# Performance work log

Hardware: AMD Instinct MI355X
Metric: run time of the kernel (lower is better)

Reference implementation:

```python
import jax, jax.numpy as jnp
import numpy as np
import math

B, S, D = 2, 2048, 1024
H, HD = 16, 64
ROT = 16          # rotary_dim = head_dim * 0.25
FF = 4096
EPS = 1e-5


def setup_inputs() -> dict:
    key = jax.random.key(0)
    ks = jax.random.split(key, 12)
    sc = lambda *sh: 0.02
    inp = {
        "x": jax.random.normal(ks[0], (B, S, D), jnp.float32),
        "attention_mask": jnp.tril(jnp.ones((S, S), bool))[None, None],  # causal [1,1,S,S]
        "W_qkv": jax.random.normal(ks[1], (3 * D, D), jnp.float32) * 0.02,
        "b_qkv": jnp.zeros((3 * D,), jnp.float32),
        "W_o": jax.random.normal(ks[2], (D, D), jnp.float32) * 0.02,
        "b_o": jnp.zeros((D,), jnp.float32),
        "ln1_w": jnp.ones((D,), jnp.float32),
        "ln1_b": jnp.zeros((D,), jnp.float32),
        "ln2_w": jnp.ones((D,), jnp.float32),
        "ln2_b": jnp.zeros((D,), jnp.float32),
        "W1": jax.random.normal(ks[3], (FF, D), jnp.float32) * 0.02,
        "b1": jnp.zeros((FF,), jnp.float32),
        "W2": jax.random.normal(ks[4], (D, FF), jnp.float32) * 0.02,
        "b2": jnp.zeros((D,), jnp.float32),
    }
    # real rotary frequencies, shaped [1,1,S,ROT//2,2]
    inv_freq = 1.0 / (10000.0 ** (jnp.arange(0, ROT, 2, dtype=jnp.float32) / ROT))
    t = jnp.arange(S, dtype=jnp.float32)
    ang = t[:, None] * inv_freq[None, :]                      # [S, ROT//2]
    inp["freqs_cis"] = jnp.stack([jnp.cos(ang), jnp.sin(ang)], -1)[None, None]
    return inp


def layer_norm(x, w, b):
    mu = jnp.mean(x, -1, keepdims=True)
    var = jnp.mean(jnp.square(x - mu), -1, keepdims=True)
    return (x - mu) * jax.lax.rsqrt(var + EPS) * w + b


def apply_rotate_emb(x, freqs_cis):
    # x: [B,H,S,ROT]; freqs_cis: [1,1,S,ROT//2,2]
    x1, x2 = x[..., : ROT // 2], x[..., ROT // 2 :]
    cos, sin = freqs_cis[..., 0], freqs_cis[..., 1]
    return jnp.concatenate([x1 * cos - x2 * sin, x1 * sin + x2 * cos], -1)


def reference(x, attention_mask, freqs_cis, W_qkv, b_qkv, W_o, b_o,
              ln1_w, ln1_b, ln2_w, ln2_b, W1, b1, W2, b2):
    h = layer_norm(x, ln1_w, ln1_b)
    qkv = jnp.einsum("bsd,ed->bse", h, W_qkv) + b_qkv
    q, k, v = jnp.split(qkv, 3, axis=-1)
    to_heads = lambda t: t.reshape(B, S, H, HD).transpose(0, 2, 1, 3)  # [B,H,S,HD]
    q, k, v = to_heads(q), to_heads(k), to_heads(v)
    q = jnp.concatenate([apply_rotate_emb(q[..., :ROT], freqs_cis), q[..., ROT:]], -1)
    k = jnp.concatenate([apply_rotate_emb(k[..., :ROT], freqs_cis), k[..., ROT:]], -1)
    scores = jnp.einsum("bhqd,bhkd->bhqk", q, k) / math.sqrt(HD)
    scores = jnp.where(attention_mask, scores, -jnp.inf)
    probs = jax.nn.softmax(scores, axis=-1)
    out = jnp.einsum("bhqk,bhkd->bhqd", probs, v)
    out = out.transpose(0, 2, 1, 3).reshape(B, S, D)
    attn_out = jnp.einsum("bsd,ed->bse", out, W_o) + b_o
    # parallel residual (dropout is identity in eval)
    h2 = layer_norm(x, ln2_w, ln2_b)
    ff = jnp.einsum("bsf,df->bsd", jax.nn.gelu(jnp.einsum("bsd,fd->bsf", h2, W1) + b1, approximate=False), W2) + b2
    return x + ff + attn_out
```

## Files before the change

kernel.cpp:

```cpp
#include <hip/hip_runtime.h>

#define DEV __device__ __forceinline__

typedef __bf16 bf16;
typedef bf16 bf16x4 __attribute__((ext_vector_type(4)));
typedef bf16 bf16x8 __attribute__((ext_vector_type(8)));
typedef float f32x4 __attribute__((ext_vector_type(4)));

DEV f32x4 mfma16(bf16x8 a, bf16x8 b, f32x4 c) {
  return __builtin_amdgcn_mfma_f32_16x16x32_bf16(a, b, c, 0, 0, 0);
}

DEV void gload_lds16(const bf16* g, bf16* l) {
  __builtin_amdgcn_global_load_lds((const __attribute__((address_space(1))) void*)g,
                                   (__attribute__((address_space(3))) void*)l, 16, 0, 0);
}

#define PH_BAR __builtin_amdgcn_s_barrier()
#define VM(NSTR) asm volatile("s_waitcnt vmcnt(" NSTR ")" ::: "memory")
#define WAITBAR(NSTR) asm volatile("s_waitcnt vmcnt(" NSTR ")\n\ts_barrier" ::: "memory")

DEV float fast_gelu(float x) {
  const float z = x * x;
  const float w = __builtin_fmaf(z, 0.1029353f, 2.3019853f);
  const float e = __builtin_amdgcn_exp2f(x * w);
  const float r = __builtin_amdgcn_rcpf(1.0f + e);
  return x - x * r;
}

__global__ __launch_bounds__(256) void ln_cast_all(
    const float* __restrict__ x,
    const float* __restrict__ ln1w, const float* __restrict__ ln1b,
    const float* __restrict__ ln2w, const float* __restrict__ ln2b,
    bf16* __restrict__ h1, bf16* __restrict__ h2,
    const float* __restrict__ Wqkv_f, const float* __restrict__ W1_f,
    const float* __restrict__ Wo_f, const float* __restrict__ W2_f,
    bf16* __restrict__ wQKV, bf16* __restrict__ w1, bf16* __restrict__ wCat)
{
  const int b = blockIdx.x, t = threadIdx.x;
  if (b < 4096) {
    __shared__ float red[2][4];
    const int lane = t & 63, wave = t >> 6;
    const float4 v = ((const float4*)(x + (size_t)b * 1024))[t];
    float vv[4] = {v.x, v.y, v.z, v.w};
    float s = vv[0] + vv[1] + vv[2] + vv[3];
    float q = vv[0]*vv[0] + vv[1]*vv[1] + vv[2]*vv[2] + vv[3]*vv[3];
    #pragma unroll
    for (int o = 32; o; o >>= 1) { s += __shfl_xor(s, o); q += __shfl_xor(q, o); }
    if (lane == 0) { red[0][wave] = s; red[1][wave] = q; }
    __syncthreads();
    s = red[0][0] + red[0][1] + red[0][2] + red[0][3];
    q = red[1][0] + red[1][1] + red[1][2] + red[1][3];
    const float mu = s * (1.0f / 1024.0f);
    const float var = q * (1.0f / 1024.0f) - mu * mu;
    const float rs = rsqrtf(var + 1e-5f);
    bf16x4 o1, o2;
    #pragma unroll
    for (int j = 0; j < 4; ++j) {
      const int i = t * 4 + j;
      const float xh = (vv[j] - mu) * rs;
      o1[j] = (bf16)(xh * ln1w[i] + ln1b[i]);
      o2[j] = (bf16)(xh * ln2w[i] + ln2b[i]);
    }
    *(bf16x4*)&h1[(size_t)b * 1024 + t * 4] = o1;
    *(bf16x4*)&h2[(size_t)b * 1024 + t * 4] = o2;
    return;
  }
  const int cb = b - 4096;
  if (cb < 3072) {
    const int i = cb * 256 + t;
    const float4 v = ((const float4*)Wqkv_f)[i];
    bf16x4 o = {(bf16)v.x, (bf16)v.y, (bf16)v.z, (bf16)v.w};
    ((bf16x4*)wQKV)[i] = o;
  } else if (cb < 7168) {
    const int i = (cb - 3072) * 256 + t;
    const float4 v = ((const float4*)W1_f)[i];
    bf16x4 o = {(bf16)v.x, (bf16)v.y, (bf16)v.z, (bf16)v.w};
    ((bf16x4*)w1)[i] = o;
  } else if (cb < 8192) {
    const int row = cb - 7168;
    const float4 v = *(const float4*)&Wo_f[(size_t)row * 1024 + t * 4];
    bf16x4 o = {(bf16)v.x, (bf16)v.y, (bf16)v.z, (bf16)v.w};
    *(bf16x4*)&wCat[(size_t)row * 5120 + t * 4] = o;
  } else {
    const int row = cb - 8192;
    #pragma unroll
    for (int k = 0; k < 4; ++k) {
      const int col = t * 4 + k * 1024;
      const float4 v = *(const float4*)&W2_f[(size_t)row * 4096 + col];
      bf16x4 o = {(bf16)v.x, (bf16)v.y, (bf16)v.z, (bf16)v.w};
      *(bf16x4*)&wCat[(size_t)row * 5120 + 1024 + col] = o;
    }
  }
}

DEV bf16x8 ldfrag(const bf16* unit, int lr, int g) {
  return *(const bf16x8*)&unit[lr * 32 + ((g ^ ((lr >> 1) & 3)) << 3)];
}
DEV void read_bfr(const bf16* unit, int blr, int g, bf16x8 bfr[4]) {
  #pragma unroll
  for (int nj = 0; nj < 4; ++nj) bfr[nj] = ldfrag(unit, blr + nj * 16, g);
}
DEV void read_af(const bf16* unit, int alr, int g, bf16x8 af[4]) {
  #pragma unroll
  for (int ml = 0; ml < 4; ++ml) af[ml] = ldfrag(unit, alr + ml * 16, g);
}
DEV void do_mfma(const bf16x8 af[4], const bf16x8 bfr[4], f32x4 acc[8][4], int mh) {
  __builtin_amdgcn_s_setprio(1);
  #pragma unroll
  for (int ml = 0; ml < 4; ++ml)
    #pragma unroll
    for (int nj = 0; nj < 4; ++nj)
      acc[mh * 4 + ml][nj] = mfma16(af[ml], bfr[nj], acc[mh * 4 + ml][nj]);
  __builtin_amdgcn_s_setprio(0);
}

template <int EPI>
__global__ __launch_bounds__(512) void gemm256(
    const bf16* __restrict__ A, const bf16* __restrict__ B,
    const float* __restrict__ bias, void* __restrict__ Cv,
    void* __restrict__ P1, void* __restrict__ P2, void* __restrict__ P3,
    int K, int ldc, int ntiles, int nbx, int nkt)
{
  __shared__ __align__(16) bf16 As[2][2][2][4096];
  __shared__ __align__(16) bf16 Bs[2][2][2][4096];
  const int tid = threadIdx.x;
  const int lane = tid & 63, wave = tid >> 6;
  const int wm = wave >> 2, wn = wave & 3;
  const int g = lane >> 4, c = lane & 15;
  const int cpx = gridDim.x >> 3;
  const int swz = ((int)blockIdx.x & 7) * cpx + ((int)blockIdx.x >> 3);
  const int tile = swz % ntiles;
  const int sk = swz / ntiles;
  const int bm = (tile / nbx) * 256, bn = (tile % nbx) * 256;

  const int slr = tid >> 2;
  const int sch = (tid & 3) ^ ((tid >> 3) & 3);
  const bf16* aU[2][2];
  const bf16* bU[2][2];
  {
    const bf16* a0 = A + (size_t)(bm + ((slr >> 6) * 128) + (slr & 63)) * K
                       + (size_t)sk * nkt * 64 + sch * 8;
    const bf16* b0 = B + (size_t)(bn + slr) * K + (size_t)sk * nkt * 64 + sch * 8;
    aU[0][0] = a0;            aU[0][1] = a0 + (size_t)64 * K;
    aU[1][0] = a0 + 32;       aU[1][1] = a0 + (size_t)64 * K + 32;
    bU[0][0] = b0;            bU[0][1] = b0 + (size_t)128 * K;
    bU[1][0] = b0 + 32;       bU[1][1] = b0 + (size_t)128 * K + 32;
  }
#define STG_A(bf_, kkh_, ub_, ko_) gload_lds16(aU[kkh_][ub_] + (ko_), &As[bf_][kkh_][ub_][wave * 512])
#define STG_B(bf_, kkh_, ub_, ko_) gload_lds16(bU[kkh_][ub_] + (ko_), &Bs[bf_][kkh_][ub_][wave * 512])

  f32x4 acc[8][4] = {};
  bf16x8 bfr[4], af[4];
  const int alr = (wm << 6) + c;
  const int blr = ((wn & 1) << 6) + c;
  const int bub = wn >> 1;

  STG_B(0, 0, 0, 0); STG_B(0, 0, 1, 0); STG_A(0, 0, 0, 0); STG_A(0, 0, 1, 0);
  STG_B(0, 1, 0, 0); STG_B(0, 1, 1, 0); STG_A(0, 1, 0, 0); STG_A(0, 1, 1, 0);
  WAITBAR("4");

  for (int t = 0; t < nkt - 1; ++t) {
    const int buf = t & 1, nxt = buf ^ 1;
    const int ko = (t + 1) * 64;
    read_bfr(&Bs[buf][0][bub][0], blr, g, bfr);
    read_af(&As[buf][0][0][0], alr, g, af);
    STG_B(nxt, 0, 0, ko); STG_B(nxt, 0, 1, ko);
    PH_BAR;
    do_mfma(af, bfr, acc, 0);
    PH_BAR;
    read_af(&As[buf][0][1][0], alr, g, af);
    STG_A(nxt, 0, 0, ko); STG_A(nxt, 0, 1, ko);
    PH_BAR;
    do_mfma(af, bfr, acc, 1);
    VM("4");
    PH_BAR;
    read_bfr(&Bs[buf][1][bub][0], blr, g, bfr);
    read_af(&As[buf][1][0][0], alr, g, af);
    STG_B(nxt, 1, 0, ko); STG_B(nxt, 1, 1, ko);
    PH_BAR;
    do_mfma(af, bfr, acc, 0);
    PH_BAR;
    read_af(&As[buf][1][1][0], alr, g, af);
    STG_A(nxt, 1, 0, ko); STG_A(nxt, 1, 1, ko);
    PH_BAR;
    do_mfma(af, bfr, acc, 1);
    VM("4");
    PH_BAR;
  }
  {
    const int buf = (nkt - 1) & 1;
    read_bfr(&Bs[buf][0][bub][0], blr, g, bfr);
    read_af(&As[buf][0][0][0], alr, g, af);
    PH_BAR;
    do_mfma(af, bfr, acc, 0);
    PH_BAR;
    read_af(&As[buf][0][1][0], alr, g, af);
    PH_BAR;
    do_mfma(af, bfr, acc, 1);
    VM("0");
    PH_BAR;
    read_bfr(&Bs[buf][1][bub][0], blr, g, bfr);
    read_af(&As[buf][1][0][0], alr, g, af);
    PH_BAR;
    do_mfma(af, bfr, acc, 0);
    PH_BAR;
    read_af(&As[buf][1][1][0], alr, g, af);
    PH_BAR;
    do_mfma(af, bfr, acc, 1);
  }
#undef STG_A
#undef STG_B

  bf16* Pp = nullptr;
  if constexpr (EPI == 2)
    Pp = (bf16*)((sk == 1) ? P1 : (sk == 2) ? P2 : (sk == 3) ? P3 : Cv);
  const int row0 = bm + wm * 128 + 4 * g;
  const int col0 = bn + wn * 64 + c;
  #pragma unroll
  for (int mi = 0; mi < 8; ++mi) {
    #pragma unroll
    for (int nj = 0; nj < 4; ++nj) {
      const int col = col0 + nj * 16;
      float bv = 0.0f;
      if constexpr (EPI < 2) bv = bias[col];
      #pragma unroll
      for (int r = 0; r < 4; ++r) {
        const size_t idx = (size_t)(row0 + mi * 16 + r) * ldc + col;
        float vo = acc[mi][nj][r] + bv;
        if constexpr (EPI == 0) {
          ((bf16*)Cv)[idx] = (bf16)vo;
        } else if constexpr (EPI == 1) {
          ((bf16*)Cv)[idx] = (bf16)fast_gelu(vo);
        } else {
          Pp[idx] = (bf16)vo;
        }
      }
    }
  }
}

__global__ __launch_bounds__(256) void combine_out(
    const bf16* __restrict__ q0, const bf16* __restrict__ q1,
    const bf16* __restrict__ q2, const bf16* __restrict__ q3,
    const float* __restrict__ x,
    const float* __restrict__ bo, const float* __restrict__ b2,
    float* __restrict__ out)
{
  const int row = blockIdx.x, t = threadIdx.x;
  const size_t base = (size_t)row * 1024 + t * 4;
  const bf16x4 a0 = *(const bf16x4*)&q0[base];
  const bf16x4 a1 = *(const bf16x4*)&q1[base];
  const bf16x4 a2 = *(const bf16x4*)&q2[base];
  const bf16x4 a3 = *(const bf16x4*)&q3[base];
  const float4 vx = *(const float4*)&x[base];
  const float4 vb = *(const float4*)&bo[t * 4];
  const float4 vc = *(const float4*)&b2[t * 4];
  float4 o;
  o.x = (float)a0[0] + (float)a1[0] + (float)a2[0] + (float)a3[0] + vx.x + vb.x + vc.x;
  o.y = (float)a0[1] + (float)a1[1] + (float)a2[1] + (float)a3[1] + vx.y + vb.y + vc.y;
  o.z = (float)a0[2] + (float)a1[2] + (float)a2[2] + (float)a3[2] + vx.z + vb.z + vc.z;
  o.w = (float)a0[3] + (float)a1[3] + (float)a2[3] + (float)a3[3] + vx.w + vb.w + vc.w;
  *(float4*)&out[base] = o;
}

__global__ __launch_bounds__(256) void rope_reshape(
    const bf16* __restrict__ qkv, const float* __restrict__ freqs,
    bf16* __restrict__ Q, bf16* __restrict__ K, bf16* __restrict__ VT)
{
  __shared__ bf16 vt[64][72];
  const int t = threadIdx.x;
  const int bh = blockIdx.y, b = bh >> 4, h = bh & 15;
  const int sc = blockIdx.x * 64;
  const int sl = t >> 2, s = sc + sl;
  const int d0 = (t & 3) * 16;

  const size_t rowbase = (size_t)(b * 2048 + s) * 3072 + h * 64 + d0;
  const size_t obase = ((size_t)bh * 2048 + s) * 64 + d0;

  #pragma unroll
  for (int which = 0; which < 2; ++which) {
    const bf16* src = qkv + rowbase + which * 1024;
    bf16x8 v0 = *(const bf16x8*)src;
    bf16x8 v1 = *(const bf16x8*)(src + 8);
    if (d0 == 0) {
      bf16x8 r0, r1;
      #pragma unroll
      for (int j = 0; j < 8; ++j) {
        const float cs = freqs[s * 16 + j * 2];
        const float sn = freqs[s * 16 + j * 2 + 1];
        const float x1 = (float)v0[j], x2 = (float)v1[j];
        r0[j] = (bf16)(x1 * cs - x2 * sn);
        r1[j] = (bf16)(x1 * sn + x2 * cs);
      }
      v0 = r0; v1 = r1;
    }
    bf16* dst = (which == 0 ? Q : K) + obase;
    *(bf16x8*)dst = v0;
    *(bf16x8*)(dst + 8) = v1;
  }
  {
    const bf16* src = qkv + rowbase + 2048;
    bf16x8 v0 = *(const bf16x8*)src;
    bf16x8 v1 = *(const bf16x8*)(src + 8);
    #pragma unroll
    for (int j = 0; j < 8; ++j) { vt[sl][d0 + j] = v0[j]; vt[sl][d0 + 8 + j] = v1[j]; }
  }
  __syncthreads();
  {
    const int d = t >> 2;
    const int s0 = (t & 3) * 16;
    bf16x8 o0, o1;
    #pragma unroll
    for (int j = 0; j < 8; ++j) { o0[j] = vt[s0 + j][d]; o1[j] = vt[s0 + 8 + j][d]; }
    bf16* dst = VT + ((size_t)bh * 64 + d) * 2048 + sc + s0;
    *(bf16x8*)dst = o0;
    *(bf16x8*)(dst + 8) = o1;
  }
}

__global__ __launch_bounds__(512, 4) void attn_kernel(
    const bf16* __restrict__ Q, const bf16* __restrict__ Kg,
    const bf16* __restrict__ VTg, bf16* __restrict__ O, int ldO)
{
  __shared__ __align__(16) bf16 Ks[4][64][64];
  __shared__ __align__(16) bf16 Vs[4][64][64];
  __shared__ __align__(16) bf16 Ps[8][16][64];

  const int tid = threadIdx.x;
  const int lane = tid & 63, wave = tid >> 6;
  const int g = lane >> 4, c = lane & 15;
  const int L = blockIdx.x;
  const int half = L >> 8, r = L & 255;
  const int bh = (half << 4) | (r >> 4);
  const int qtile = half ? (15 - (r & 15)) : (r & 15);
  const int qw = qtile * 128 + wave * 16;

  const bf16* Qp = Q + (size_t)bh * 2048 * 64;
  const bf16* Kp = Kg + (size_t)bh * 2048 * 64;
  const bf16* Vp = VTg + (size_t)bh * 64 * 2048;

  const int srow = lane >> 3;
  const int schunk = (lane & 7) ^ srow;
  const int svr = wave * 8 + srow;
  const size_t kdelta = (size_t)64 * 64;

  bf16x8 qreg[2];
  {
    const float qs = 0.125f * 1.44269504f;
    bf16x8 t0 = *(const bf16x8*)&Qp[(size_t)(qw + c) * 64 + g * 8];
    bf16x8 t1 = *(const bf16x8*)&Qp[(size_t)(qw + c) * 64 + 32 + g * 8];
    #pragma unroll
    for (int j = 0; j < 8; ++j) {
      qreg[0][j] = (bf16)((float)t0[j] * qs);
      qreg[1][j] = (bf16)((float)t1[j] * qs);
    }
  }
  bf16x8 ones;
  #pragma unroll
  for (int j = 0; j < 8; ++j) ones[j] = (bf16)1.0f;

  const int cq = c & 7;
  int fo[4][2];
  #pragma unroll
  for (int i = 0; i < 4; ++i)
    #pragma unroll
    for (int kk = 0; kk < 2; ++kk)
      fo[i][kk] = (i * 16 + c) * 64 + (((kk * 4 + g) ^ cq) << 3);
  bf16* pw[4];
  #pragma unroll
  for (int kf = 0; kf < 4; ++kf)
    pw[kf] = &Ps[wave][c][((((kf * 2 + (g >> 1)) ^ cq) << 3)) + ((g & 1) << 2)];
  const bf16* pr[2];
  #pragma unroll
  for (int kk = 0; kk < 2; ++kk)
    pr[kk] = &Ps[wave][c][((kk * 4 + g) ^ cq) << 3];
  const bf16* ks0 = &Ks[0][0][0];
  const bf16* vs0 = &Vs[0][0][0];

  f32x4 oacc[4] = {};
  f32x4 lacc = {};
  float m_ = -1e30f;

  const int nkb = 2 * qtile + 2;
#define STAGE(j_) do { const int b4_ = (j_) & 3;                                   \
    gload_lds16(&Kp[(size_t)((j_) * 64 + svr) * 64 + schunk * 8], &Ks[b4_][wave * 8][0]); \
    gload_lds16(&Vp[(size_t)svr * 2048 + (j_) * 64 + schunk * 8], &Vs[b4_][wave * 8][0]); \
  } while (0)

  auto qkt = [&](f32x4* st, int bufi) {
    const bf16* kt = ks0 + bufi * kdelta;
    __builtin_amdgcn_s_setprio(1);
    #pragma unroll
    for (int kf = 0; kf < 4; ++kf) {
      f32x4 z = {};
      z = mfma16(*(const bf16x8*)(kt + fo[kf][0]), qreg[0], z);
      st[kf] = mfma16(*(const bf16x8*)(kt + fo[kf][1]), qreg[1], z);
    }
    __builtin_amdgcn_s_setprio(0);
  };

  auto smpv = [&](const f32x4* st, int j_, int bufi) {
    const int kbase = j_ * 64;
    float v[16];
    if (kbase + 63 > qw) {
      const int qrel = qw + c - kbase;
      #pragma unroll
      for (int kf = 0; kf < 4; ++kf)
        #pragma unroll
        for (int rr = 0; rr < 4; ++rr)
          v[kf * 4 + rr] = (kf * 16 + 4 * g + rr <= qrel) ? st[kf][rr] : -1e30f;
    } else {
      #pragma unroll
      for (int kf = 0; kf < 4; ++kf)
        #pragma unroll
        for (int rr = 0; rr < 4; ++rr)
          v[kf * 4 + rr] = st[kf][rr];
    }
    float u0 = fmaxf(fmaxf(v[0], v[1]), v[2]);
    float u1 = fmaxf(fmaxf(v[3], v[4]), v[5]);
    float u2 = fmaxf(fmaxf(v[6], v[7]), v[8]);
    float u3 = fmaxf(fmaxf(v[9], v[10]), v[11]);
    float u4 = fmaxf(fmaxf(v[12], v[13]), v[14]);
    float tm = fmaxf(fmaxf(fmaxf(u0, u1), u2), fmaxf(fmaxf(u3, u4), v[15]));
    if (__any(tm > m_ + 8.0f)) {
      float tr = fmaxf(tm, __shfl_xor(tm, 16));
      tr = fmaxf(tr, __shfl_xor(tr, 32));
      const float mn = fmaxf(m_, tr);
      const float alpha = __builtin_amdgcn_exp2f(m_ - mn);
      m_ = mn;
      lacc[0] *= alpha; lacc[1] *= alpha; lacc[2] *= alpha; lacc[3] *= alpha;
      #pragma unroll
      for (int df = 0; df < 4; ++df) {
        oacc[df][0] *= alpha; oacc[df][1] *= alpha;
        oacc[df][2] *= alpha; oacc[df][3] *= alpha;
      }
    }
    bf16 p[16];
    #pragma unroll
    for (int i = 0; i < 16; ++i)
      p[i] = (bf16)__builtin_amdgcn_exp2f(v[i] - m_);
    #pragma unroll
    for (int kf = 0; kf < 4; ++kf) {
      bf16x4 pk = {p[kf * 4], p[kf * 4 + 1], p[kf * 4 + 2], p[kf * 4 + 3]};
      *(bf16x4*)pw[kf] = pk;
    }
    bf16x8 pfrag0 = *(const bf16x8*)pr[0];
    bf16x8 pfrag1 = *(const bf16x8*)pr[1];
    const bf16* vt = vs0 + bufi * kdelta;
    __builtin_amdgcn_s_setprio(1);
    #pragma unroll
    for (int df = 0; df < 4; ++df) {
      oacc[df] = mfma16(*(const bf16x8*)(vt + fo[df][0]), pfrag0, oacc[df]);
      oacc[df] = mfma16(*(const bf16x8*)(vt + fo[df][1]), pfrag1, oacc[df]);
    }
    lacc = mfma16(ones, pfrag0, lacc);
    lacc = mfma16(ones, pfrag1, lacc);
    __builtin_amdgcn_s_setprio(0);
  };

  f32x4 stA[4], stB[4];
  STAGE(0); STAGE(1); STAGE(2);
  VM("2");
  PH_BAR;
  qkt(stA, 0);

  const int nit = nkb >> 1;
  for (int i = 0; i < nit; ++i) {
    const int jA = 2 * i, jB = 2 * i + 1;
    const bool stgA = (jA + 3 < nkb);
    if (stgA) STAGE(jA + 3);
    if (jB * 64 <= qw + 15) qkt(stB, jB & 3);
    smpv(stA, jA, jA & 3);
    if (stgA) { VM("2"); } else { VM("0"); }
    PH_BAR;
    const bool stgB = (jB + 3 < nkb);
    if (stgB) STAGE(jB + 3);
    if (jB + 1 < nkb && (jB + 1) * 64 <= qw + 15) qkt(stA, (jB + 1) & 3);
    if (jB * 64 <= qw + 15) smpv(stB, jB, jB & 3);
    if (stgB) { VM("2"); } else { VM("0"); }
    PH_BAR;
  }
#undef STAGE

  const int b = bh >> 4, h = bh & 15;
  const float inv = 1.0f / lacc[0];
  const int s = qw + c;
  #pragma unroll
  for (int df = 0; df < 4; ++df) {
    bf16x4 o;
    #pragma unroll
    for (int rr = 0; rr < 4; ++rr) o[rr] = (bf16)(oacc[df][rr] * inv);
    *(bf16x4*)&O[(size_t)(b * 2048 + s) * ldO + h * 64 + df * 16 + 4 * g] = o;
  }
}

extern "C" void kernel_launch(void* const* d_in, const int* in_sizes, int n_in,
                              void* d_out, int out_size, void* d_ws, size_t ws_size,
                              hipStream_t stream) {
  const float* x     = (const float*)d_in[0];
  const float* W_qkv = (const float*)d_in[2];
  const float* b_qkv = (const float*)d_in[3];
  const float* W_o   = (const float*)d_in[4];
  const float* b_o   = (const float*)d_in[5];
  const float* ln1w  = (const float*)d_in[6];
  const float* ln1b  = (const float*)d_in[7];
  const float* ln2w  = (const float*)d_in[8];
  const float* ln2b  = (const float*)d_in[9];
  const float* W1    = (const float*)d_in[10];
  const float* b1    = (const float*)d_in[11];
  const float* W2    = (const float*)d_in[12];
  const float* b2    = (const float*)d_in[13];
  const float* freqs = (const float*)d_in[14];
  float* out = (float*)d_out;

  char* ws = (char*)d_ws;
  const size_t MB = (size_t)1 << 20;
  bf16* h1   = (bf16*)(ws + 0 * MB);
  bf16* h2   = (bf16*)(ws + 8 * MB);
  bf16* wQKV = (bf16*)(ws + 16 * MB);
  bf16* wCat = (bf16*)(ws + 22 * MB);
  bf16* w1   = (bf16*)(ws + 32 * MB);
  bf16* qkv  = (bf16*)(ws + 40 * MB);
  bf16* Qb   = (bf16*)(ws + 64 * MB);
  bf16* Kb   = (bf16*)(ws + 72 * MB);
  bf16* VTb  = (bf16*)(ws + 80 * MB);
  bf16* A2   = (bf16*)(ws + 88 * MB);
  bf16* q0   = (bf16*)(ws + 0 * MB);
  bf16* q1   = (bf16*)(ws + 8 * MB);
  bf16* q2   = (bf16*)(ws + 40 * MB);
  bf16* q3   = (bf16*)(ws + 48 * MB);

  ln_cast_all<<<13312, 256, 0, stream>>>(x, ln1w, ln1b, ln2w, ln2b, h1, h2,
                                         W_qkv, W1, W_o, W2, wQKV, w1, wCat);

  gemm256<0><<<192, 512, 0, stream>>>(h1, wQKV, b_qkv, qkv,
                                      nullptr, nullptr, nullptr,
                                      1024, 3072, 192, 12, 16);
  rope_reshape<<<dim3(32, 32), 256, 0, stream>>>(qkv, freqs, Qb, Kb, VTb);
  attn_kernel<<<512, 512, 0, stream>>>(Qb, Kb, VTb, A2, 5120);
  gemm256<1><<<256, 512, 0, stream>>>(h2, w1, b1, A2 + 1024,
                                      nullptr, nullptr, nullptr,
                                      1024, 5120, 256, 16, 16);
  gemm256<2><<<256, 512, 0, stream>>>(A2, wCat, nullptr, q0,
                                      q1, q2, q3,
                                      5120, 1024, 64, 4, 20);
  combine_out<<<4096, 256, 0, stream>>>(q0, q1, q2, q3, x, b_o, b2, out);
}
```

Baseline: 196.4 us.

## Merge QKV and FFN-up GEMMs into one launch; widen attention blocks

The QKV projection and the FFN up-projection GEMMs become a single 448-block launch that picks its operands and epilogue (bias, or bias plus GELU) per block segment. This fills more CUs at once and drops a launch and a tail. The attention kernel moves from 512-thread blocks over 128 query rows to 1024-thread blocks over 256 query rows, with K and V staging split between the two thread halves. The change risks load imbalance, since causal work now varies more per block and there are only 256 attention blocks, and it adds pressure on registers and LDS.

```diff
diff --git a/kernel.cpp b/kernel.cpp
--- a/kernel.cpp
+++ b/kernel.cpp
@@ -115,11 +115,142 @@
   __builtin_amdgcn_s_setprio(0);
 }
 
-template <int EPI>
-__global__ __launch_bounds__(512) void gemm256(
+DEV void gemm_kloop(bf16 (*As)[2][2][4096], bf16 (*Bs)[2][2][4096],
+                    const bf16* aU[2][2], const bf16* bU[2][2],
+                    int wave, int alr, int blr, int bub, int g, int nkt,
+                    f32x4 acc[8][4])
+{
+  bf16x8 bfr[4], af[4];
+#define STG_A(bf_, kkh_, ub_, ko_) gload_lds16(aU[kkh_][ub_] + (ko_), &As[bf_][kkh_][ub_][wave * 512])
+#define STG_B(bf_, kkh_, ub_, ko_) gload_lds16(bU[kkh_][ub_] + (ko_), &Bs[bf_][kkh_][ub_][wave * 512])
+  STG_B(0, 0, 0, 0); STG_B(0, 0, 1, 0); STG_A(0, 0, 0, 0); STG_A(0, 0, 1, 0);
+  STG_B(0, 1, 0, 0); STG_B(0, 1, 1, 0); STG_A(0, 1, 0, 0); STG_A(0, 1, 1, 0);
+  WAITBAR("4");
+
+  for (int t = 0; t < nkt - 1; ++t) {
+    const int buf = t & 1, nxt = buf ^ 1;
+    const int ko = (t + 1) * 64;
+    read_bfr(&Bs[buf][0][bub][0], blr, g, bfr);
+    read_af(&As[buf][0][0][0], alr, g, af);
+    STG_B(nxt, 0, 0, ko); STG_B(nxt, 0, 1, ko);
+    PH_BAR;
+    do_mfma(af, bfr, acc, 0);
+    PH_BAR;
+    read_af(&As[buf][0][1][0], alr, g, af);
+    STG_A(nxt, 0, 0, ko); STG_A(nxt, 0, 1, ko);
+    PH_BAR;
+    do_mfma(af, bfr, acc, 1);
+    VM("4");
+    PH_BAR;
+    read_bfr(&Bs[buf][1][bub][0], blr, g, bfr);
+    read_af(&As[buf][1][0][0], alr, g, af);
+    STG_B(nxt, 1, 0, ko); STG_B(nxt, 1, 1, ko);
+    PH_BAR;
+    do_mfma(af, bfr, acc, 0);
+    PH_BAR;
+    read_af(&As[buf][1][1][0], alr, g, af);
+    STG_A(nxt, 1, 0, ko); STG_A(nxt, 1, 1, ko);
+    PH_BAR;
+    do_mfma(af, bfr, acc, 1);
+    VM("4");
+    PH_BAR;
+  }
+  {
+    const int buf = (nkt - 1) & 1;
+    read_bfr(&Bs[buf][0][bub][0], blr, g, bfr);
+    read_af(&As[buf][0][0][0], alr, g, af);
+    PH_BAR;
+    do_mfma(af, bfr, acc, 0);
+    PH_BAR;
+    read_af(&As[buf][0][1][0], alr, g, af);
+    PH_BAR;
+    do_mfma(af, bfr, acc, 1);
+    VM("0");
+    PH_BAR;
+    read_bfr(&Bs[buf][1][bub][0], blr, g, bfr);
+    read_af(&As[buf][1][0][0], alr, g, af);
+    PH_BAR;
+    do_mfma(af, bfr, acc, 0);
+    PH_BAR;
+    read_af(&As[buf][1][1][0], alr, g, af);
+    PH_BAR;
+    do_mfma(af, bfr, acc, 1);
+  }
+#undef STG_A
+#undef STG_B
+}
+
+__global__ __launch_bounds__(512) void gemm_dual(
+    const bf16* __restrict__ A0, const bf16* __restrict__ B0,
+    const float* __restrict__ bias0, bf16* __restrict__ C0,
+    const bf16* __restrict__ A1, const bf16* __restrict__ B1,
+    const float* __restrict__ bias1, bf16* __restrict__ C1)
+{
+  __shared__ __align__(16) bf16 As[2][2][2][4096];
+  __shared__ __align__(16) bf16 Bs[2][2][2][4096];
+  const int tid = threadIdx.x;
+  const int lane = tid & 63, wave = tid >> 6;
+  const int wm = wave >> 2, wn = wave & 3;
+  const int g = lane >> 4, c = lane & 15;
+
+  const int bid = blockIdx.x;
+  const int seg = (bid >= 192);
+  const int nseg = seg ? 256 : 192;
+  const int nbx  = seg ? 16 : 12;
+  const int ldc  = seg ? 5120 : 3072;
+  const bf16* A = seg ? A1 : A0;
+  const bf16* B = seg ? B1 : B0;
+  const float* bias = seg ? bias1 : bias0;
+  bf16* C = seg ? C1 : C0;
+  const int K = 1024, nkt = 16;
+
+  const int bs = bid - (seg ? 192 : 0);
+  const int cpx = nseg >> 3;
+  const int swz = (bs & 7) * cpx + (bs >> 3);
+  const int bm = (swz / nbx) * 256, bn = (swz % nbx) * 256;
+
+  const int slr = tid >> 2;
+  const int sch = (tid & 3) ^ ((tid >> 3) & 3);
+  const bf16* aU[2][2];
+  const bf16* bU[2][2];
+  {
+    const bf16* a0 = A + (size_t)(bm + ((slr >> 6) * 128) + (slr & 63)) * K + sch * 8;
+    const bf16* b0 = B + (size_t)(bn + slr) * K + sch * 8;
+    aU[0][0] = a0;            aU[0][1] = a0 + (size_t)64 * K;
+    aU[1][0] = a0 + 32;       aU[1][1] = a0 + (size_t)64 * K + 32;
+    bU[0][0] = b0;            bU[0][1] = b0 + (size_t)128 * K;
+    bU[1][0] = b0 + 32;       bU[1][1] = b0 + (size_t)128 * K + 32;
+  }
+
+  f32x4 acc[8][4] = {};
+  const int alr = (wm << 6) + c;
+  const int blr = ((wn & 1) << 6) + c;
+  const int bub = wn >> 1;
+
+  gemm_kloop(As, Bs, aU, bU, wave, alr, blr, bub, g, nkt, acc);
+
+  const int row0 = bm + wm * 128 + 4 * g;
+  const int col0 = bn + wn * 64 + c;
+  #pragma unroll
+  for (int mi = 0; mi < 8; ++mi) {
+    #pragma unroll
+    for (int nj = 0; nj < 4; ++nj) {
+      const int col = col0 + nj * 16;
+      const float bv = bias[col];
+      #pragma unroll
+      for (int r = 0; r < 4; ++r) {
+        const size_t idx = (size_t)(row0 + mi * 16 + r) * ldc + col;
+        const float vo = acc[mi][nj][r] + bv;
+        C[idx] = (bf16)(seg ? fast_gelu(vo) : vo);
+      }
+    }
+  }
+}
+
+__global__ __launch_bounds__(512) void gemm_splitk(
     const bf16* __restrict__ A, const bf16* __restrict__ B,
-    const float* __restrict__ bias, void* __restrict__ Cv,
-    void* __restrict__ P1, void* __restrict__ P2, void* __restrict__ P3,
+    bf16* __restrict__ P0, bf16* __restrict__ P1,
+    bf16* __restrict__ P2, bf16* __restrict__ P3,
     int K, int ldc, int ntiles, int nbx, int nkt)
 {
   __shared__ __align__(16) bf16 As[2][2][2][4096];
@@ -147,74 +278,15 @@
     bU[0][0] = b0;            bU[0][1] = b0 + (size_t)128 * K;
     bU[1][0] = b0 + 32;       bU[1][1] = b0 + (size_t)128 * K + 32;
   }
-#define STG_A(bf_, kkh_, ub_, ko_) gload_lds16(aU[kkh_][ub_] + (ko_), &As[bf_][kkh_][ub_][wave * 512])
-#define STG_B(bf_, kkh_, ub_, ko_) gload_lds16(bU[kkh_][ub_] + (ko_), &Bs[bf_][kkh_][ub_][wave * 512])
 
   f32x4 acc[8][4] = {};
-  bf16x8 bfr[4], af[4];
   const int alr = (wm << 6) + c;
   const int blr = ((wn & 1) << 6) + c;
   const int bub = wn >> 1;
 
-  STG_B(0, 0, 0, 0); STG_B(0, 0, 1, 0); STG_A(0, 0, 0, 0); STG_A(0, 0, 1, 0);
-  STG_B(0, 1, 0, 0); STG_B(0, 1, 1, 0); STG_A(0, 1, 0, 0); STG_A(0, 1, 1, 0);
-  WAITBAR("4");
-
-  for (int t = 0; t < nkt - 1; ++t) {
-    const int buf = t & 1, nxt = buf ^ 1;
-    const int ko = (t + 1) * 64;
-    read_bfr(&Bs[buf][0][bub][0], blr, g, bfr);
-    read_af(&As[buf][0][0][0], alr, g, af);
-    STG_B(nxt, 0, 0, ko); STG_B(nxt, 0, 1, ko);
-    PH_BAR;
-    do_mfma(af, bfr, acc, 0);
-    PH_BAR;
-    read_af(&As[buf][0][1][0], alr, g, af);
-    STG_A(nxt, 0, 0, ko); STG_A(nxt, 0, 1, ko);
-    PH_BAR;
-    do_mfma(af, bfr, acc, 1);
-    VM("4");
-    PH_BAR;
-    read_bfr(&Bs[buf][1][bub][0], blr, g, bfr);
-    read_af(&As[buf][1][0][0], alr, g, af);
-    STG_B(nxt, 1, 0, ko); STG_B(nxt, 1, 1, ko);
-    PH_BAR;
-    do_mfma(af, bfr, acc, 0);
-    PH_BAR;
-    read_af(&As[buf][1][1][0], alr, g, af);
-    STG_A(nxt, 1, 0, ko); STG_A(nxt, 1, 1, ko);
-    PH_BAR;
-    do_mfma(af, bfr, acc, 1);
-    VM("4");
-    PH_BAR;
-  }
-  {
-    const int buf = (nkt - 1) & 1;
-    read_bfr(&Bs[buf][0][bub][0], blr, g, bfr);
-    read_af(&As[buf][0][0][0], alr, g, af);
-    PH_BAR;
-    do_mfma(af, bfr, acc, 0);
-    PH_BAR;
-    read_af(&As[buf][0][1][0], alr, g, af);
-    PH_BAR;
-    do_mfma(af, bfr, acc, 1);
-    VM("0");
-    PH_BAR;
-    read_bfr(&Bs[buf][1][bub][0], blr, g, bfr);
-    read_af(&As[buf][1][0][0], alr, g, af);
-    PH_BAR;
-    do_mfma(af, bfr, acc, 0);
-    PH_BAR;
-    read_af(&As[buf][1][1][0], alr, g, af);
-    PH_BAR;
-    do_mfma(af, bfr, acc, 1);
-  }
-#undef STG_A
-#undef STG_B
-
-  bf16* Pp = nullptr;
-  if constexpr (EPI == 2)
-    Pp = (bf16*)((sk == 1) ? P1 : (sk == 2) ? P2 : (sk == 3) ? P3 : Cv);
+  gemm_kloop(As, Bs, aU, bU, wave, alr, blr, bub, g, nkt, acc);
+
+  bf16* Pp = (sk == 1) ? P1 : (sk == 2) ? P2 : (sk == 3) ? P3 : P0;
   const int row0 = bm + wm * 128 + 4 * g;
   const int col0 = bn + wn * 64 + c;
   #pragma unroll
@@ -222,19 +294,10 @@
     #pragma unroll
     for (int nj = 0; nj < 4; ++nj) {
       const int col = col0 + nj * 16;
-      float bv = 0.0f;
-      if constexpr (EPI < 2) bv = bias[col];
       #pragma unroll
       for (int r = 0; r < 4; ++r) {
         const size_t idx = (size_t)(row0 + mi * 16 + r) * ldc + col;
-        float vo = acc[mi][nj][r] + bv;
-        if constexpr (EPI == 0) {
-          ((bf16*)Cv)[idx] = (bf16)vo;
-        } else if constexpr (EPI == 1) {
-          ((bf16*)Cv)[idx] = (bf16)fast_gelu(vo);
-        } else {
-          Pp[idx] = (bf16)vo;
-        }
+        Pp[idx] = (bf16)acc[mi][nj][r];
       }
     }
   }
@@ -319,30 +382,29 @@
   }
 }
 
-__global__ __launch_bounds__(512, 4) void attn_kernel(
+__global__ __launch_bounds__(1024, 4) void attn_kernel(
     const bf16* __restrict__ Q, const bf16* __restrict__ Kg,
     const bf16* __restrict__ VTg, bf16* __restrict__ O, int ldO)
 {
   __shared__ __align__(16) bf16 Ks[4][64][64];
   __shared__ __align__(16) bf16 Vs[4][64][64];
-  __shared__ __align__(16) bf16 Ps[8][16][64];
+  __shared__ __align__(16) bf16 Ps[16][16][64];
 
   const int tid = threadIdx.x;
   const int lane = tid & 63, wave = tid >> 6;
   const int g = lane >> 4, c = lane & 15;
   const int L = blockIdx.x;
-  const int half = L >> 8, r = L & 255;
-  const int bh = (half << 4) | (r >> 4);
-  const int qtile = half ? (15 - (r & 15)) : (r & 15);
-  const int qw = qtile * 128 + wave * 16;
+  const int bh = L >> 3, p = L & 7;
+  const int qw = p * 256 + wave * 16;
 
   const bf16* Qp = Q + (size_t)bh * 2048 * 64;
   const bf16* Kp = Kg + (size_t)bh * 2048 * 64;
   const bf16* Vp = VTg + (size_t)bh * 64 * 2048;
 
+  const int stw = (tid >> 6) & 7;
   const int srow = lane >> 3;
   const int schunk = (lane & 7) ^ srow;
-  const int svr = wave * 8 + srow;
+  const int svr = stw * 8 + srow;
   const size_t kdelta = (size_t)64 * 64;
 
   bf16x8 qreg[2];
@@ -382,10 +444,12 @@
   f32x4 lacc = {};
   float m_ = -1e30f;
 
-  const int nkb = 2 * qtile + 2;
-#define STAGE(j_) do { const int b4_ = (j_) & 3;                                   \
-    gload_lds16(&Kp[(size_t)((j_) * 64 + svr) * 64 + schunk * 8], &Ks[b4_][wave * 8][0]); \
-    gload_lds16(&Vp[(size_t)svr * 2048 + (j_) * 64 + schunk * 8], &Vs[b4_][wave * 8][0]); \
+  const int nkb = 4 * p + 4;
+#define STAGE(j_) do { const int b4_ = (j_) & 3;                                     \
+    if (tid < 512)                                                                   \
+      gload_lds16(&Kp[(size_t)((j_) * 64 + svr) * 64 + schunk * 8], &Ks[b4_][stw * 8][0]); \
+    else                                                                             \
+      gload_lds16(&Vp[(size_t)svr * 2048 + (j_) * 64 + schunk * 8], &Vs[b4_][stw * 8][0]); \
   } while (0)
 
   auto qkt = [&](f32x4* st, int bufi) {
@@ -436,13 +500,13 @@
         oacc[df][2] *= alpha; oacc[df][3] *= alpha;
       }
     }
-    bf16 p[16];
+    bf16 pq[16];
     #pragma unroll
     for (int i = 0; i < 16; ++i)
-      p[i] = (bf16)__builtin_amdgcn_exp2f(v[i] - m_);
+      pq[i] = (bf16)__builtin_amdgcn_exp2f(v[i] - m_);
     #pragma unroll
     for (int kf = 0; kf < 4; ++kf) {
-      bf16x4 pk = {p[kf * 4], p[kf * 4 + 1], p[kf * 4 + 2], p[kf * 4 + 3]};
+      bf16x4 pk = {pq[kf * 4], pq[kf * 4 + 1], pq[kf * 4 + 2], pq[kf * 4 + 3]};
       *(bf16x4*)pw[kf] = pk;
     }
     bf16x8 pfrag0 = *(const bf16x8*)pr[0];
@@ -461,7 +525,7 @@
 
   f32x4 stA[4], stB[4];
   STAGE(0); STAGE(1); STAGE(2);
-  VM("2");
+  VM("1");
   PH_BAR;
   qkt(stA, 0);
 
@@ -471,14 +535,14 @@
     const bool stgA = (jA + 3 < nkb);
     if (stgA) STAGE(jA + 3);
     if (jB * 64 <= qw + 15) qkt(stB, jB & 3);
-    smpv(stA, jA, jA & 3);
-    if (stgA) { VM("2"); } else { VM("0"); }
+    if (jA * 64 <= qw + 15) smpv(stA, jA, jA & 3);
+    if (stgA) { VM("1"); } else { VM("0"); }
     PH_BAR;
     const bool stgB = (jB + 3 < nkb);
     if (stgB) STAGE(jB + 3);
     if (jB + 1 < nkb && (jB + 1) * 64 <= qw + 15) qkt(stA, (jB + 1) & 3);
     if (jB * 64 <= qw + 15) smpv(stB, jB, jB & 3);
-    if (stgB) { VM("2"); } else { VM("0"); }
+    if (stgB) { VM("1"); } else { VM("0"); }
     PH_BAR;
   }
 #undef STAGE
@@ -533,17 +597,11 @@
 
   ln_cast_all<<<13312, 256, 0, stream>>>(x, ln1w, ln1b, ln2w, ln2b, h1, h2,
                                          W_qkv, W1, W_o, W2, wQKV, w1, wCat);
-
-  gemm256<0><<<192, 512, 0, stream>>>(h1, wQKV, b_qkv, qkv,
-                                      nullptr, nullptr, nullptr,
-                                      1024, 3072, 192, 12, 16);
+  gemm_dual<<<448, 512, 0, stream>>>(h1, wQKV, b_qkv, qkv,
+                                     h2, w1, b1, A2 + 1024);
   rope_reshape<<<dim3(32, 32), 256, 0, stream>>>(qkv, freqs, Qb, Kb, VTb);
-  attn_kernel<<<512, 512, 0, stream>>>(Qb, Kb, VTb, A2, 5120);
-  gemm256<1><<<256, 512, 0, stream>>>(h2, w1, b1, A2 + 1024,
-                                      nullptr, nullptr, nullptr,
-                                      1024, 5120, 256, 16, 16);
-  gemm256<2><<<256, 512, 0, stream>>>(A2, wCat, nullptr, q0,
-                                      q1, q2, q3,
-                                      5120, 1024, 64, 4, 20);
+  attn_kernel<<<256, 1024, 0, stream>>>(Qb, Kb, VTb, A2, 5120);
+  gemm_splitk<<<256, 512, 0, stream>>>(A2, wCat, q0, q1, q2, q3,
+                                       5120, 1024, 64, 4, 20);
   combine_out<<<4096, 256, 0, stream>>>(q0, q1, q2, q3, x, b_o, b2, out);
 }
```

Result: slower. 204.0 us (+3.8%).

## Use 1024-thread attention blocks covering 256 queries with split K/V staging

Applied to the files above, without the earlier changes.

The attention kernel now launches 256 blocks of 16 waves, each covering 256 query rows, instead of 512 blocks of 8 waves with paired q-tiles for causal balance. K and V staging is split so the first half of the threads loads K and the second half loads V, which changes the vmcnt waits. A guard skips fully masked softmax/PV steps per wave. The GEMM k-loop is also moved into a helper function. The new mapping drops the causal load-balancing pairing, so later query blocks do much more work than early ones, and the larger blocks may limit occupancy.

```diff
diff --git a/kernel.cpp b/kernel.cpp
--- a/kernel.cpp
+++ b/kernel.cpp
@@ -115,6 +115,71 @@
   __builtin_amdgcn_s_setprio(0);
 }
 
+DEV void gemm_kloop(bf16 (*As)[2][2][4096], bf16 (*Bs)[2][2][4096],
+                    const bf16* aU[2][2], const bf16* bU[2][2],
+                    int wave, int alr, int blr, int bub, int g, int nkt,
+                    f32x4 acc[8][4])
+{
+  bf16x8 bfr[4], af[4];
+#define STG_A(bf_, kkh_, ub_, ko_) gload_lds16(aU[kkh_][ub_] + (ko_), &As[bf_][kkh_][ub_][wave * 512])
+#define STG_B(bf_, kkh_, ub_, ko_) gload_lds16(bU[kkh_][ub_] + (ko_), &Bs[bf_][kkh_][ub_][wave * 512])
+  STG_B(0, 0, 0, 0); STG_B(0, 0, 1, 0); STG_A(0, 0, 0, 0); STG_A(0, 0, 1, 0);
+  STG_B(0, 1, 0, 0); STG_B(0, 1, 1, 0); STG_A(0, 1, 0, 0); STG_A(0, 1, 1, 0);
+  WAITBAR("4");
+
+  for (int t = 0; t < nkt - 1; ++t) {
+    const int buf = t & 1, nxt = buf ^ 1;
+    const int ko = (t + 1) * 64;
+    read_bfr(&Bs[buf][0][bub][0], blr, g, bfr);
+    read_af(&As[buf][0][0][0], alr, g, af);
+    STG_B(nxt, 0, 0, ko); STG_B(nxt, 0, 1, ko);
+    PH_BAR;
+    do_mfma(af, bfr, acc, 0);
+    PH_BAR;
+    read_af(&As[buf][0][1][0], alr, g, af);
+    STG_A(nxt, 0, 0, ko); STG_A(nxt, 0, 1, ko);
+    PH_BAR;
+    do_mfma(af, bfr, acc, 1);
+    VM("4");
+    PH_BAR;
+    read_bfr(&Bs[buf][1][bub][0], blr, g, bfr);
+    read_af(&As[buf][1][0][0], alr, g, af);
+    STG_B(nxt, 1, 0, ko); STG_B(nxt, 1, 1, ko);
+    PH_BAR;
+    do_mfma(af, bfr, acc, 0);
+    PH_BAR;
+    read_af(&As[buf][1][1][0], alr, g, af);
+    STG_A(nxt, 1, 0, ko); STG_A(nxt, 1, 1, ko);
+    PH_BAR;
+    do_mfma(af, bfr, acc, 1);
+    VM("4");
+    PH_BAR;
+  }
+  {
+    const int buf = (nkt - 1) & 1;
+    read_bfr(&Bs[buf][0][bub][0], blr, g, bfr);
+    read_af(&As[buf][0][0][0], alr, g, af);
+    PH_BAR;
+    do_mfma(af, bfr, acc, 0);
+    PH_BAR;
+    read_af(&As[buf][0][1][0], alr, g, af);
+    PH_BAR;
+    do_mfma(af, bfr, acc, 1);
+    VM("0");
+    PH_BAR;
+    read_bfr(&Bs[buf][1][bub][0], blr, g, bfr);
+    read_af(&As[buf][1][0][0], alr, g, af);
+    PH_BAR;
+    do_mfma(af, bfr, acc, 0);
+    PH_BAR;
+    read_af(&As[buf][1][1][0], alr, g, af);
+    PH_BAR;
+    do_mfma(af, bfr, acc, 1);
+  }
+#undef STG_A
+#undef STG_B
+}
+
 template <int EPI>
 __global__ __launch_bounds__(512) void gemm256(
     const bf16* __restrict__ A, const bf16* __restrict__ B,
@@ -147,70 +212,13 @@
     bU[0][0] = b0;            bU[0][1] = b0 + (size_t)128 * K;
     bU[1][0] = b0 + 32;       bU[1][1] = b0 + (size_t)128 * K + 32;
   }
-#define STG_A(bf_, kkh_, ub_, ko_) gload_lds16(aU[kkh_][ub_] + (ko_), &As[bf_][kkh_][ub_][wave * 512])
-#define STG_B(bf_, kkh_, ub_, ko_) gload_lds16(bU[kkh_][ub_] + (ko_), &Bs[bf_][kkh_][ub_][wave * 512])
 
   f32x4 acc[8][4] = {};
-  bf16x8 bfr[4], af[4];
   const int alr = (wm << 6) + c;
   const int blr = ((wn & 1) << 6) + c;
   const int bub = wn >> 1;
 
-  STG_B(0, 0, 0, 0); STG_B(0, 0, 1, 0); STG_A(0, 0, 0, 0); STG_A(0, 0, 1, 0);
-  STG_B(0, 1, 0, 0); STG_B(0, 1, 1, 0); STG_A(0, 1, 0, 0); STG_A(0, 1, 1, 0);
-  WAITBAR("4");
-
-  for (int t = 0; t < nkt - 1; ++t) {
-    const int buf = t & 1, nxt = buf ^ 1;
-    const int ko = (t + 1) * 64;
-    read_bfr(&Bs[buf][0][bub][0], blr, g, bfr);
-    read_af(&As[buf][0][0][0], alr, g, af);
-    STG_B(nxt, 0, 0, ko); STG_B(nxt, 0, 1, ko);
-    PH_BAR;
-    do_mfma(af, bfr, acc, 0);
-    PH_BAR;
-    read_af(&As[buf][0][1][0], alr, g, af);
-    STG_A(nxt, 0, 0, ko); STG_A(nxt, 0, 1, ko);
-    PH_BAR;
-    do_mfma(af, bfr, acc, 1);
-    VM("4");
-    PH_BAR;
-    read_bfr(&Bs[buf][1][bub][0], blr, g, bfr);
-    read_af(&As[buf][1][0][0], alr, g, af);
-    STG_B(nxt, 1, 0, ko); STG_B(nxt, 1, 1, ko);
-    PH_BAR;
-    do_mfma(af, bfr, acc, 0);
-    PH_BAR;
-    read_af(&As[buf][1][1][0], alr, g, af);
-    STG_A(nxt, 1, 0, ko); STG_A(nxt, 1, 1, ko);
-    PH_BAR;
-    do_mfma(af, bfr, acc, 1);
-    VM("4");
-    PH_BAR;
-  }
-  {
-    const int buf = (nkt - 1) & 1;
-    read_bfr(&Bs[buf][0][bub][0], blr, g, bfr);
-    read_af(&As[buf][0][0][0], alr, g, af);
-    PH_BAR;
-    do_mfma(af, bfr, acc, 0);
-    PH_BAR;
-    read_af(&As[buf][0][1][0], alr, g, af);
-    PH_BAR;
-    do_mfma(af, bfr, acc, 1);
-    VM("0");
-    PH_BAR;
-    read_bfr(&Bs[buf][1][bub][0], blr, g, bfr);
-    read_af(&As[buf][1][0][0], alr, g, af);
-    PH_BAR;
-    do_mfma(af, bfr, acc, 0);
-    PH_BAR;
-    read_af(&As[buf][1][1][0], alr, g, af);
-    PH_BAR;
-    do_mfma(af, bfr, acc, 1);
-  }
-#undef STG_A
-#undef STG_B
+  gemm_kloop(As, Bs, aU, bU, wave, alr, blr, bub, g, nkt, acc);
 
   bf16* Pp = nullptr;
   if constexpr (EPI == 2)
@@ -319,30 +327,29 @@
   }
 }
 
-__global__ __launch_bounds__(512, 4) void attn_kernel(
+__global__ __launch_bounds__(1024, 4) void attn_kernel(
     const bf16* __restrict__ Q, const bf16* __restrict__ Kg,
     const bf16* __restrict__ VTg, bf16* __restrict__ O, int ldO)
 {
   __shared__ __align__(16) bf16 Ks[4][64][64];
   __shared__ __align__(16) bf16 Vs[4][64][64];
-  __shared__ __align__(16) bf16 Ps[8][16][64];
+  __shared__ __align__(16) bf16 Ps[16][16][64];
 
   const int tid = threadIdx.x;
   const int lane = tid & 63, wave = tid >> 6;
   const int g = lane >> 4, c = lane & 15;
   const int L = blockIdx.x;
-  const int half = L >> 8, r = L & 255;
-  const int bh = (half << 4) | (r >> 4);
-  const int qtile = half ? (15 - (r & 15)) : (r & 15);
-  const int qw = qtile * 128 + wave * 16;
+  const int bh = L >> 3, p = L & 7;
+  const int qw = p * 256 + wave * 16;
 
   const bf16* Qp = Q + (size_t)bh * 2048 * 64;
   const bf16* Kp = Kg + (size_t)bh * 2048 * 64;
   const bf16* Vp = VTg + (size_t)bh * 64 * 2048;
 
+  const int stw = (tid >> 6) & 7;
   const int srow = lane >> 3;
   const int schunk = (lane & 7) ^ srow;
-  const int svr = wave * 8 + srow;
+  const int svr = stw * 8 + srow;
   const size_t kdelta = (size_t)64 * 64;
 
   bf16x8 qreg[2];
@@ -382,10 +389,12 @@
   f32x4 lacc = {};
   float m_ = -1e30f;
 
-  const int nkb = 2 * qtile + 2;
-#define STAGE(j_) do { const int b4_ = (j_) & 3;                                   \
-    gload_lds16(&Kp[(size_t)((j_) * 64 + svr) * 64 + schunk * 8], &Ks[b4_][wave * 8][0]); \
-    gload_lds16(&Vp[(size_t)svr * 2048 + (j_) * 64 + schunk * 8], &Vs[b4_][wave * 8][0]); \
+  const int nkb = 4 * p + 4;
+#define STAGE(j_) do { const int b4_ = (j_) & 3;                                     \
+    if (tid < 512)                                                                   \
+      gload_lds16(&Kp[(size_t)((j_) * 64 + svr) * 64 + schunk * 8], &Ks[b4_][stw * 8][0]); \
+    else                                                                             \
+      gload_lds16(&Vp[(size_t)svr * 2048 + (j_) * 64 + schunk * 8], &Vs[b4_][stw * 8][0]); \
   } while (0)
 
   auto qkt = [&](f32x4* st, int bufi) {
@@ -436,13 +445,13 @@
         oacc[df][2] *= alpha; oacc[df][3] *= alpha;
       }
     }
-    bf16 p[16];
+    bf16 pq[16];
     #pragma unroll
     for (int i = 0; i < 16; ++i)
-      p[i] = (bf16)__builtin_amdgcn_exp2f(v[i] - m_);
+      pq[i] = (bf16)__builtin_amdgcn_exp2f(v[i] - m_);
     #pragma unroll
     for (int kf = 0; kf < 4; ++kf) {
-      bf16x4 pk = {p[kf * 4], p[kf * 4 + 1], p[kf * 4 + 2], p[kf * 4 + 3]};
+      bf16x4 pk = {pq[kf * 4], pq[kf * 4 + 1], pq[kf * 4 + 2], pq[kf * 4 + 3]};
       *(bf16x4*)pw[kf] = pk;
     }
     bf16x8 pfrag0 = *(const bf16x8*)pr[0];
@@ -461,7 +470,7 @@
 
   f32x4 stA[4], stB[4];
   STAGE(0); STAGE(1); STAGE(2);
-  VM("2");
+  VM("1");
   PH_BAR;
   qkt(stA, 0);
 
@@ -471,14 +480,14 @@
     const bool stgA = (jA + 3 < nkb);
     if (stgA) STAGE(jA + 3);
     if (jB * 64 <= qw + 15) qkt(stB, jB & 3);
-    smpv(stA, jA, jA & 3);
-    if (stgA) { VM("2"); } else { VM("0"); }
+    if (jA * 64 <= qw + 15) smpv(stA, jA, jA & 3);
+    if (stgA) { VM("1"); } else { VM("0"); }
     PH_BAR;
     const bool stgB = (jB + 3 < nkb);
     if (stgB) STAGE(jB + 3);
     if (jB + 1 < nkb && (jB + 1) * 64 <= qw + 15) qkt(stA, (jB + 1) & 3);
     if (jB * 64 <= qw + 15) smpv(stB, jB, jB & 3);
-    if (stgB) { VM("2"); } else { VM("0"); }
+    if (stgB) { VM("1"); } else { VM("0"); }
     PH_BAR;
   }
 #undef STAGE
@@ -533,12 +542,11 @@
 
   ln_cast_all<<<13312, 256, 0, stream>>>(x, ln1w, ln1b, ln2w, ln2b, h1, h2,
                                          W_qkv, W1, W_o, W2, wQKV, w1, wCat);
-
   gemm256<0><<<192, 512, 0, stream>>>(h1, wQKV, b_qkv, qkv,
                                       nullptr, nullptr, nullptr,
                                       1024, 3072, 192, 12, 16);
   rope_reshape<<<dim3(32, 32), 256, 0, stream>>>(qkv, freqs, Qb, Kb, VTb);
-  attn_kernel<<<512, 512, 0, stream>>>(Qb, Kb, VTb, A2, 5120);
+  attn_kernel<<<256, 1024, 0, stream>>>(Qb, Kb, VTb, A2, 5120);
   gemm256<1><<<256, 512, 0, stream>>>(h2, w1, b1, A2 + 1024,
                                       nullptr, nullptr, nullptr,
                                       1024, 5120, 256, 16, 16);
```

After: 202.1 us. 2.9% more time.
